# Kernel optimization log

Measured on AMD Instinct MI355X. Metric: run time of the kernel, lower is better.

Reference implementation:

```python
import jax, jax.numpy as jnp
import numpy as np

NEG_INF = -1e9
ALPHA = 0.2  # LeakyReLU slope


def gat_layer(x, adj, W, a_src, a_dst):
    # x: (N, F), adj: (N, N) bool, W: (F, H, D), a_src/a_dst: (H, D)
    h = jnp.einsum('nf,fhd->nhd', x, W)                 # (N, H, D)
    es = jnp.einsum('nhd,hd->nh', h, a_src)             # score from target node i
    ed = jnp.einsum('nhd,hd->nh', h, a_dst)             # score from neighbor j
    e = jax.nn.leaky_relu(es[:, None, :] + ed[None, :, :], ALPHA)  # (N, N, H)
    e = jnp.where(adj[:, :, None], e, NEG_INF)
    attn = jax.nn.softmax(e, axis=1)                    # softmax over neighbors j
    out = jnp.einsum('ijh,jhd->ihd', attn, h)           # (N, H, D)
    N, H, D = out.shape
    return out.reshape(N, H * D)                        # concat heads


def setup_inputs() -> dict:
    key = jax.random.key(0)
    ks = jax.random.split(key, 8)
    N, F, H1, D1, C = 4096, 512, 8, 8, 16
    node_matrix = jax.random.normal(ks[0], (N, F), dtype=jnp.float32)
    adj = jax.random.bernoulli(ks[1], 0.005, (N, N))
    adj = jnp.logical_or(adj, jnp.eye(N, dtype=bool))   # self-loops
    s1 = 1.0 / np.sqrt(F)
    s2 = 1.0 / np.sqrt(H1 * D1)
    return {
        'node_matrix': node_matrix,
        'adj_matrix': adj,
        'W1': jax.random.normal(ks[2], (F, H1, D1), dtype=jnp.float32) * s1,
        'a1_src': jax.random.normal(ks[3], (H1, D1), dtype=jnp.float32) * s1,
        'a1_dst': jax.random.normal(ks[4], (H1, D1), dtype=jnp.float32) * s1,
        'W2': jax.random.normal(ks[5], (H1 * D1, 1, C), dtype=jnp.float32) * s2,
        'a2_src': jax.random.normal(ks[6], (1, C), dtype=jnp.float32) * s2,
        'a2_dst': jax.random.normal(ks[7], (1, C), dtype=jnp.float32) * s2,
    }


def reference(node_matrix, adj_matrix, W1, a1_src, a1_dst, W2, a2_src, a2_dst):
    # dropout layers are identity in eval mode
    z1 = gat_layer(node_matrix, adj_matrix, W1, a1_src, a1_dst)  # (N, 64)
    a1 = jax.nn.elu(z1)
    z2 = gat_layer(a1, adj_matrix, W2, a2_src, a2_dst)           # (N, num_classes)
    return z2
```

## Files before the change

kernel.cpp:

```cpp
#include <hip/hip_runtime.h>

#define N_NODES 4096
#define F_IN    512
#define NH1     8
#define F1      64
#define C2      16
#define MAXDEG  128

#define GEMM_BLKS (N_NODES / 8)
#define SCAN_BLKS (N_NODES / 4)

__device__ __forceinline__ float wave_sum(float v) {
    for (int o = 32; o >= 1; o >>= 1) v += __shfl_xor(v, o, 64);
    return v;
}

__global__ void detect_width_kernel(const unsigned char* __restrict__ adj,
                                    int* __restrict__ flag) {
    __shared__ unsigned int cnts[4];
    __shared__ unsigned int mxv;
    int t = threadIdx.x;
    if (t < 4) cnts[t] = 0u;
    if (t == 0) mxv = 0u;
    __syncthreads();
    unsigned int c0 = 0, c1 = 0, c2 = 0, c3 = 0, m = 0;
    const uint4* p = (const uint4*)(adj) + t * 16;
    #pragma unroll
    for (int i = 0; i < 16; ++i) {
        uint4 q = p[i];
        unsigned int wd[4] = {q.x, q.y, q.z, q.w};
        #pragma unroll
        for (int k = 0; k < 4; ++k) {
            unsigned int v = wd[k];
            unsigned int b0 = v & 0xffu, b1 = (v >> 8) & 0xffu;
            unsigned int b2 = (v >> 16) & 0xffu, b3 = (v >> 24) & 0xffu;
            if (b0) { c0++; m = m > b0 ? m : b0; }
            if (b1) { c1++; m = m > b1 ? m : b1; }
            if (b2) { c2++; m = m > b2 ? m : b2; }
            if (b3) { c3++; m = m > b3 ? m : b3; }
        }
    }
    atomicAdd(&cnts[0], c0); atomicAdd(&cnts[1], c1);
    atomicAdd(&cnts[2], c2); atomicAdd(&cnts[3], c3);
    atomicMax(&mxv, m);
    __syncthreads();
    if (t == 0) {
        int w;
        if (cnts[1] + cnts[2] + cnts[3] == 0u)      w = 4;
        else if (cnts[0] == 0u && cnts[1] == 0u)    w = 4;
        else if (cnts[0] == 0u && cnts[2] == 0u)    w = 2;
        else if (mxv <= 1u)                          w = 1;
        else                                         w = 2;
        *flag = w;
    }
}

__global__ __launch_bounds__(256) void frontend_kernel(
        const unsigned char* __restrict__ adj, const int* __restrict__ flag,
        unsigned short* __restrict__ neigh, int* __restrict__ deg,
        const float* __restrict__ x, const float* __restrict__ W1,
        const float* __restrict__ asrc, const float* __restrict__ adst,
        float* __restrict__ h1, float* __restrict__ es, float* __restrict__ ed) {
    __shared__ __align__(16) float smem[4096 + 2 * 4096];
    __shared__ int scnt[4];
    const int t = threadIdx.x;
    const int wv = t >> 6;
    const int l = t & 63;

    if (blockIdx.x < GEMM_BLKS) {
        float* xs  = smem;
        float* wt0 = smem + 4096;
        float* wt1 = smem + 8192;
        const int row0 = blockIdx.x * 8;

        {
            const float4* src = (const float4*)(x + (size_t)row0 * F_IN);
            float4* dst = (float4*)xs;
            #pragma unroll
            for (int i = 0; i < 4; ++i) dst[t + i * 256] = src[t + i * 256];
        }
        const float4* w1v = (const float4*)W1;
        {
            float4* d = (float4*)wt0;
            #pragma unroll
            for (int i = 0; i < 4; ++i) d[t + i * 256] = w1v[t + i * 256];
        }

        const int c = t & 63;
        const int rq = t >> 6;
        float a0 = 0.f, a1 = 0.f;
        float* wcur = wt0;
        float* wnxt = wt1;
        for (int tile = 0; tile < 8; ++tile) {
            __syncthreads();
            float4 pf0, pf1, pf2, pf3;
            if (tile < 7) {
                const float4* s = w1v + (size_t)(tile + 1) * 1024;
                pf0 = s[t]; pf1 = s[t + 256]; pf2 = s[t + 512]; pf3 = s[t + 768];
            }
            const float4* xr0 = (const float4*)&xs[rq * F_IN + tile * 64];
            const float4* xr1 = (const float4*)&xs[(rq + 4) * F_IN + tile * 64];
            #pragma unroll
            for (int kk = 0; kk < 64; kk += 4) {
                float4 x0 = xr0[kk >> 2];
                float4 x1 = xr1[kk >> 2];
                float w0 = wcur[(kk + 0) * 64 + c];
                float w1 = wcur[(kk + 1) * 64 + c];
                float w2 = wcur[(kk + 2) * 64 + c];
                float w3 = wcur[(kk + 3) * 64 + c];
                a0 += x0.x * w0 + x0.y * w1 + x0.z * w2 + x0.w * w3;
                a1 += x1.x * w0 + x1.y * w1 + x1.z * w2 + x1.w * w3;
            }
            if (tile < 7) {
                float4* d = (float4*)wnxt;
                d[t] = pf0; d[t + 256] = pf1; d[t + 512] = pf2; d[t + 768] = pf3;
            }
            float* tmp = wcur; wcur = wnxt; wnxt = tmp;
        }

        const int n0 = row0 + rq;
        h1[(size_t)n0 * F1 + c] = a0;
        h1[(size_t)(n0 + 4) * F1 + c] = a1;
        float s0 = a0 * asrc[c], d0 = a0 * adst[c];
        float s1 = a1 * asrc[c], d1 = a1 * adst[c];
        s0 += __shfl_xor(s0, 1); s0 += __shfl_xor(s0, 2); s0 += __shfl_xor(s0, 4);
        d0 += __shfl_xor(d0, 1); d0 += __shfl_xor(d0, 2); d0 += __shfl_xor(d0, 4);
        s1 += __shfl_xor(s1, 1); s1 += __shfl_xor(s1, 2); s1 += __shfl_xor(s1, 4);
        d1 += __shfl_xor(d1, 1); d1 += __shfl_xor(d1, 2); d1 += __shfl_xor(d1, 4);
        if ((c & 7) == 0) {
            es[n0 * NH1 + (c >> 3)] = s0;
            ed[n0 * NH1 + (c >> 3)] = d0;
            es[(n0 + 4) * NH1 + (c >> 3)] = s1;
            ed[(n0 + 4) * NH1 + (c >> 3)] = d1;
        }
    } else {
        const int row = (blockIdx.x - GEMM_BLKS) * 4 + wv;
        int* cnt = scnt + wv;
        if (l == 0) *cnt = 0;
        const int w = *flag;
        unsigned short* outp = neigh + (size_t)row * MAXDEG;
        if (w == 1) {
            const uint4* p = (const uint4*)(adj + (size_t)row * N_NODES);
            uint4 v[4];
            #pragma unroll
            for (int i = 0; i < 4; ++i) v[i] = p[l + 64 * i];
            #pragma unroll
            for (int i = 0; i < 4; ++i) {
                if ((v[i].x | v[i].y | v[i].z | v[i].w) == 0u) continue;
                unsigned int wd[4] = {v[i].x, v[i].y, v[i].z, v[i].w};
                int base = (l + 64 * i) * 16;
                for (int q = 0; q < 4; ++q) {
                    unsigned int word = wd[q];
                    for (int bb = 0; bb < 4; ++bb) {
                        if ((word >> (8 * bb)) & 0xffu) {
                            int pos = atomicAdd(cnt, 1);
                            if (pos < MAXDEG) outp[pos] = (unsigned short)(base + q * 4 + bb);
                        }
                    }
                }
            }
        } else if (w == 2) {
            const uint4* p = (const uint4*)(adj + (size_t)row * N_NODES * 2);
            uint4 v[8];
            #pragma unroll
            for (int i = 0; i < 8; ++i) v[i] = p[l + 64 * i];
            #pragma unroll
            for (int i = 0; i < 8; ++i) {
                if ((v[i].x | v[i].y | v[i].z | v[i].w) == 0u) continue;
                unsigned int wd[4] = {v[i].x, v[i].y, v[i].z, v[i].w};
                int base = (l + 64 * i) * 8;
                for (int q = 0; q < 4; ++q) {
                    unsigned int word = wd[q];
                    if (word & 0xffffu) {
                        int pos = atomicAdd(cnt, 1);
                        if (pos < MAXDEG) outp[pos] = (unsigned short)(base + q * 2);
                    }
                    if (word >> 16) {
                        int pos = atomicAdd(cnt, 1);
                        if (pos < MAXDEG) outp[pos] = (unsigned short)(base + q * 2 + 1);
                    }
                }
            }
        } else {
            const uint4* p = (const uint4*)(adj + (size_t)row * N_NODES * 4);
            #pragma unroll
            for (int b = 0; b < 2; ++b) {
                uint4 v[8];
                #pragma unroll
                for (int i = 0; i < 8; ++i) v[i] = p[l + 64 * (b * 8 + i)];
                #pragma unroll
                for (int i = 0; i < 8; ++i) {
                    if ((v[i].x | v[i].y | v[i].z | v[i].w) == 0u) continue;
                    unsigned int wd[4] = {v[i].x, v[i].y, v[i].z, v[i].w};
                    int base = (l + 64 * (b * 8 + i)) * 4;
                    for (int q = 0; q < 4; ++q) {
                        if (wd[q]) {
                            int pos = atomicAdd(cnt, 1);
                            if (pos < MAXDEG) outp[pos] = (unsigned short)(base + q);
                        }
                    }
                }
            }
        }
        if (l == 0) deg[row] = min(*cnt, MAXDEG);
    }
}

__global__ __launch_bounds__(256) void attn1_kernel(
        const unsigned short* __restrict__ neigh, const int* __restrict__ deg,
        const float* __restrict__ h1, const float* __restrict__ es,
        const float* __restrict__ ed, const float* __restrict__ W2,
        const float* __restrict__ a2s, const float* __restrict__ a2d,
        float* __restrict__ h2, float* __restrict__ es2, float* __restrict__ ed2) {
    __shared__ unsigned short listA[4 * MAXDEG];
    __shared__ float arowA[4 * 64];
    __shared__ float pbufA[4 * 576];
    const int t = threadIdx.x;
    const int wv = t >> 6;
    const int l = t & 63;
    const int i = blockIdx.x * 4 + wv;
    unsigned short* list = listA + wv * MAXDEG;
    float* arow = arowA + wv * 64;
    float* pw   = pbufA + wv * 576;
    const int hq = l >> 3;

    const int K = deg[i];
    const unsigned short* lst = neigh + (size_t)i * MAXDEG;
    for (int j = l; j < MAXDEG; j += 64) list[j] = (j < K) ? lst[j] : (unsigned short)0;
    __builtin_amdgcn_wave_barrier();

    float plsum[NH1];
    #pragma unroll
    for (int h = 0; h < NH1; ++h) plsum[h] = 0.f;
    const float4 e0 = *(const float4*)(es + (size_t)i * NH1);
    const float4 e1 = *(const float4*)(es + (size_t)i * NH1 + 4);
    const float esi[NH1] = {e0.x, e0.y, e0.z, e0.w, e1.x, e1.y, e1.z, e1.w};
    float acc = 0.f;

    for (int t0 = 0; t0 < K; t0 += 64) {
        const int tc = min(64, K - t0);
        const bool valid = l < tc;
        const int j = valid ? (int)list[t0 + l] : 0;
        const float4 d0 = *(const float4*)(ed + (size_t)j * NH1);
        const float4 d1 = *(const float4*)(ed + (size_t)j * NH1 + 4);
        const float edv[NH1] = {d0.x, d0.y, d0.z, d0.w, d1.x, d1.y, d1.z, d1.w};
        #pragma unroll
        for (int h = 0; h < NH1; ++h) {
            float v = esi[h] + edv[h];
            v = (v >= 0.f) ? v : 0.2f * v;
            float p = valid ? __expf(v) : 0.f;
            plsum[h] += p;
            pw[l * 9 + h] = p;
        }
        __builtin_amdgcn_wave_barrier();
        const int tcPad = (tc + 7) & ~7;
        for (int u = 0; u < tcPad; u += 8) {
            #pragma unroll
            for (int vv = 0; vv < 8; ++vv) {
                int jn = (int)list[t0 + u + vv];
                acc += pw[(u + vv) * 9 + hq] * h1[(size_t)jn * F1 + l];
            }
        }
        __builtin_amdgcn_wave_barrier();
    }
    float lsum[NH1];
    #pragma unroll
    for (int h = 0; h < NH1; ++h) lsum[h] = wave_sum(plsum[h]);
    float o = acc / lsum[hq];
    float a1v = (o > 0.f) ? o : (__expf(o) - 1.f);

    arow[l] = a1v;
    __builtin_amdgcn_wave_barrier();
    const int cc = l & 15;
    const int kg = l >> 4;
    float hacc = 0.f;
    #pragma unroll
    for (int k = 0; k < 16; ++k)
        hacc += arow[kg * 16 + k] * W2[(kg * 16 + k) * C2 + cc];
    hacc += __shfl_xor(hacc, 16);
    hacc += __shfl_xor(hacc, 32);
    if (l < C2) h2[(size_t)i * C2 + l] = hacc;
    float s2 = hacc * a2s[cc];
    float d2 = hacc * a2d[cc];
    s2 += __shfl_xor(s2, 1); s2 += __shfl_xor(s2, 2);
    s2 += __shfl_xor(s2, 4); s2 += __shfl_xor(s2, 8);
    d2 += __shfl_xor(d2, 1); d2 += __shfl_xor(d2, 2);
    d2 += __shfl_xor(d2, 4); d2 += __shfl_xor(d2, 8);
    if (l == 0) { es2[i] = s2; ed2[i] = d2; }
}

__global__ __launch_bounds__(256) void attn2_kernel(
        const unsigned short* __restrict__ neigh, const int* __restrict__ deg,
        const float* __restrict__ h2, const float* __restrict__ es2,
        const float* __restrict__ ed2, float* __restrict__ out) {
    __shared__ unsigned short listA[4 * MAXDEG];
    __shared__ float pbufA[4 * 64];
    const int t = threadIdx.x;
    const int wv = t >> 6;
    const int l = t & 63;
    const int i = blockIdx.x * 4 + wv;
    unsigned short* list = listA + wv * MAXDEG;
    float* pb = pbufA + wv * 64;
    const int c = l & 15;
    const int g = l >> 4;

    const int K = deg[i];
    const unsigned short* lst = neigh + (size_t)i * MAXDEG;
    for (int j = l; j < MAXDEG; j += 64) list[j] = (j < K) ? lst[j] : (unsigned short)0;
    __builtin_amdgcn_wave_barrier();

    float plsum = 0.f, acc = 0.f;
    const float esi = es2[i];
    for (int t0 = 0; t0 < K; t0 += 64) {
        const int tc = min(64, K - t0);
        const bool valid = l < tc;
        const int j = valid ? (int)list[t0 + l] : 0;
        float v = esi + ed2[j];
        v = (v >= 0.f) ? v : 0.2f * v;
        float p = valid ? __expf(v) : 0.f;
        plsum += p;
        pb[l] = p;
        __builtin_amdgcn_wave_barrier();
        const int tcPad = (tc + 3) & ~3;
        for (int u = g; u < tcPad; u += 4) {
            int jn = (int)list[t0 + u];
            acc += pb[u] * h2[(size_t)jn * C2 + c];
        }
        __builtin_amdgcn_wave_barrier();
    }
    float lsum = wave_sum(plsum);
    acc += __shfl_xor(acc, 16);
    acc += __shfl_xor(acc, 32);
    if (l < C2) out[(size_t)i * C2 + l] = acc / lsum;
}

extern "C" void kernel_launch(void* const* d_in, const int* in_sizes, int n_in,
                              void* d_out, int out_size, void* d_ws, size_t ws_size,
                              hipStream_t stream) {
    const float* x           = (const float*)d_in[0];
    const unsigned char* adj = (const unsigned char*)d_in[1];
    const float* W1          = (const float*)d_in[2];
    const float* a1src       = (const float*)d_in[3];
    const float* a1dst       = (const float*)d_in[4];
    const float* W2          = (const float*)d_in[5];
    const float* a2src       = (const float*)d_in[6];
    const float* a2dst       = (const float*)d_in[7];
    float* out = (float*)d_out;

    char* ws = (char*)d_ws;
    size_t off = 0;
    int* flag = (int*)(ws + off);                 off += 256;
    unsigned short* neigh = (unsigned short*)(ws + off);
    off += (size_t)N_NODES * MAXDEG * 2;
    int* deg = (int*)(ws + off);                  off += (size_t)N_NODES * 4;
    float* h1 = (float*)(ws + off);               off += (size_t)N_NODES * F1 * 4;
    float* es1 = (float*)(ws + off);              off += (size_t)N_NODES * NH1 * 4;
    float* ed1 = (float*)(ws + off);              off += (size_t)N_NODES * NH1 * 4;
    float* h2 = (float*)(ws + off);               off += (size_t)N_NODES * C2 * 4;
    float* es2 = (float*)(ws + off);              off += (size_t)N_NODES * 4;
    float* ed2 = (float*)(ws + off);              off += (size_t)N_NODES * 4;

    hipLaunchKernelGGL(detect_width_kernel, dim3(1), dim3(256), 0, stream, adj, flag);
    hipLaunchKernelGGL(frontend_kernel, dim3(GEMM_BLKS + SCAN_BLKS), dim3(256), 0, stream,
                       adj, flag, neigh, deg, x, W1, a1src, a1dst, h1, es1, ed1);
    hipLaunchKernelGGL(attn1_kernel, dim3(N_NODES / 4), dim3(256), 0, stream,
                       neigh, deg, h1, es1, ed1, W2, a2src, a2dst, h2, es2, ed2);
    hipLaunchKernelGGL(attn2_kernel, dim3(N_NODES / 4), dim3(256), 0, stream,
                       neigh, deg, h2, es2, ed2, out);
}
```

Baseline: 145.9 us.

## Fold width detection into scan waves, widen GEMM tile, use shuffles for neighbor lists

Removes the separate single-block width-detection kernel. Each scan wave now redoes the detection itself by reading the first 4 KB of adj with wave votes, which saves one launch and its serialization at the cost of redundant reads. The GEMM blocks now handle 16 rows each, reusing each W tile across more rows, and use a single W buffer with an extra barrier instead of double buffering. The attention kernels drop their LDS copies of the neighbor list and broadcast indices and weights with __shfl, removing LDS traffic and wave barriers.

```diff
diff --git a/kernel.cpp b/kernel.cpp
--- a/kernel.cpp
+++ b/kernel.cpp
@@ -7,90 +7,72 @@
 #define C2      16
 #define MAXDEG  128
 
-#define GEMM_BLKS (N_NODES / 8)
-#define SCAN_BLKS (N_NODES / 4)
+#define GEMM_BLKS 256
+#define SCAN_BLKS 1024
 
 __device__ __forceinline__ float wave_sum(float v) {
     for (int o = 32; o >= 1; o >>= 1) v += __shfl_xor(v, o, 64);
     return v;
 }
 
-__global__ void detect_width_kernel(const unsigned char* __restrict__ adj,
-                                    int* __restrict__ flag) {
-    __shared__ unsigned int cnts[4];
-    __shared__ unsigned int mxv;
-    int t = threadIdx.x;
-    if (t < 4) cnts[t] = 0u;
-    if (t == 0) mxv = 0u;
-    __syncthreads();
-    unsigned int c0 = 0, c1 = 0, c2 = 0, c3 = 0, m = 0;
-    const uint4* p = (const uint4*)(adj) + t * 16;
+__device__ __forceinline__ int detect_width_wave(const unsigned char* __restrict__ adj,
+                                                 int l) {
+    bool nz0 = false, nz1 = false, nz2 = false, nz3 = false;
+    unsigned int mx = 0u;
+    const uint4* p = (const uint4*)adj;
     #pragma unroll
-    for (int i = 0; i < 16; ++i) {
-        uint4 q = p[i];
+    for (int i = 0; i < 4; ++i) {
+        uint4 q = p[l + 64 * i];
         unsigned int wd[4] = {q.x, q.y, q.z, q.w};
         #pragma unroll
         for (int k = 0; k < 4; ++k) {
             unsigned int v = wd[k];
             unsigned int b0 = v & 0xffu, b1 = (v >> 8) & 0xffu;
             unsigned int b2 = (v >> 16) & 0xffu, b3 = (v >> 24) & 0xffu;
-            if (b0) { c0++; m = m > b0 ? m : b0; }
-            if (b1) { c1++; m = m > b1 ? m : b1; }
-            if (b2) { c2++; m = m > b2 ? m : b2; }
-            if (b3) { c3++; m = m > b3 ? m : b3; }
+            if (b0) { nz0 = true; mx = mx > b0 ? mx : b0; }
+            if (b1) { nz1 = true; mx = mx > b1 ? mx : b1; }
+            if (b2) { nz2 = true; mx = mx > b2 ? mx : b2; }
+            if (b3) { nz3 = true; mx = mx > b3 ? mx : b3; }
         }
     }
-    atomicAdd(&cnts[0], c0); atomicAdd(&cnts[1], c1);
-    atomicAdd(&cnts[2], c2); atomicAdd(&cnts[3], c3);
-    atomicMax(&mxv, m);
-    __syncthreads();
-    if (t == 0) {
-        int w;
-        if (cnts[1] + cnts[2] + cnts[3] == 0u)      w = 4;
-        else if (cnts[0] == 0u && cnts[1] == 0u)    w = 4;
-        else if (cnts[0] == 0u && cnts[2] == 0u)    w = 2;
-        else if (mxv <= 1u)                          w = 1;
-        else                                         w = 2;
-        *flag = w;
-    }
+    const bool a0 = __any(nz0), a1 = __any(nz1), a2 = __any(nz2), a3 = __any(nz3);
+    const bool big = __any(mx > 1u);
+    if (!a1 && !a2 && !a3) return 4;
+    if (!a0 && !a1)        return 4;
+    if (!a0 && !a2)        return 2;
+    if (!big)              return 1;
+    return 2;
 }
 
 __global__ __launch_bounds__(256) void frontend_kernel(
-        const unsigned char* __restrict__ adj, const int* __restrict__ flag,
+        const unsigned char* __restrict__ adj,
         unsigned short* __restrict__ neigh, int* __restrict__ deg,
         const float* __restrict__ x, const float* __restrict__ W1,
         const float* __restrict__ asrc, const float* __restrict__ adst,
         float* __restrict__ h1, float* __restrict__ es, float* __restrict__ ed) {
-    __shared__ __align__(16) float smem[4096 + 2 * 4096];
+    __shared__ __align__(16) float smem[8192 + 4096];
     __shared__ int scnt[4];
     const int t = threadIdx.x;
     const int wv = t >> 6;
     const int l = t & 63;
 
     if (blockIdx.x < GEMM_BLKS) {
-        float* xs  = smem;
-        float* wt0 = smem + 4096;
-        float* wt1 = smem + 8192;
-        const int row0 = blockIdx.x * 8;
-
+        float* xs = smem;
+        float* wt = smem + 8192;
+        const int row0 = blockIdx.x * 16;
         {
             const float4* src = (const float4*)(x + (size_t)row0 * F_IN);
             float4* dst = (float4*)xs;
             #pragma unroll
-            for (int i = 0; i < 4; ++i) dst[t + i * 256] = src[t + i * 256];
+            for (int i = 0; i < 8; ++i) dst[t + i * 256] = src[t + i * 256];
         }
         const float4* w1v = (const float4*)W1;
-        {
-            float4* d = (float4*)wt0;
-            #pragma unroll
-            for (int i = 0; i < 4; ++i) d[t + i * 256] = w1v[t + i * 256];
-        }
-
-        const int c = t & 63;
-        const int rq = t >> 6;
-        float a0 = 0.f, a1 = 0.f;
-        float* wcur = wt0;
-        float* wnxt = wt1;
+        float4* wtv = (float4*)wt;
+        #pragma unroll
+        for (int i = 0; i < 4; ++i) wtv[t + i * 256] = w1v[t + i * 256];
+
+        const int c = l;
+        float a0 = 0.f, a1 = 0.f, a2 = 0.f, a3 = 0.f;
         for (int tile = 0; tile < 8; ++tile) {
             __syncthreads();
             float4 pf0, pf1, pf2, pf3;
@@ -98,46 +80,50 @@
                 const float4* s = w1v + (size_t)(tile + 1) * 1024;
                 pf0 = s[t]; pf1 = s[t + 256]; pf2 = s[t + 512]; pf3 = s[t + 768];
             }
-            const float4* xr0 = (const float4*)&xs[rq * F_IN + tile * 64];
-            const float4* xr1 = (const float4*)&xs[(rq + 4) * F_IN + tile * 64];
+            const float4* xr0 = (const float4*)&xs[(wv     ) * F_IN + tile * 64];
+            const float4* xr1 = (const float4*)&xs[(wv +  4) * F_IN + tile * 64];
+            const float4* xr2 = (const float4*)&xs[(wv +  8) * F_IN + tile * 64];
+            const float4* xr3 = (const float4*)&xs[(wv + 12) * F_IN + tile * 64];
             #pragma unroll
             for (int kk = 0; kk < 64; kk += 4) {
                 float4 x0 = xr0[kk >> 2];
                 float4 x1 = xr1[kk >> 2];
-                float w0 = wcur[(kk + 0) * 64 + c];
-                float w1 = wcur[(kk + 1) * 64 + c];
-                float w2 = wcur[(kk + 2) * 64 + c];
-                float w3 = wcur[(kk + 3) * 64 + c];
+                float4 x2 = xr2[kk >> 2];
+                float4 x3 = xr3[kk >> 2];
+                float w0 = wt[(kk + 0) * 64 + c];
+                float w1 = wt[(kk + 1) * 64 + c];
+                float w2 = wt[(kk + 2) * 64 + c];
+                float w3 = wt[(kk + 3) * 64 + c];
                 a0 += x0.x * w0 + x0.y * w1 + x0.z * w2 + x0.w * w3;
                 a1 += x1.x * w0 + x1.y * w1 + x1.z * w2 + x1.w * w3;
-            }
+                a2 += x2.x * w0 + x2.y * w1 + x2.z * w2 + x2.w * w3;
+                a3 += x3.x * w0 + x3.y * w1 + x3.z * w2 + x3.w * w3;
+            }
+            __syncthreads();
             if (tile < 7) {
-                float4* d = (float4*)wnxt;
-                d[t] = pf0; d[t + 256] = pf1; d[t + 512] = pf2; d[t + 768] = pf3;
-            }
-            float* tmp = wcur; wcur = wnxt; wnxt = tmp;
-        }
-
-        const int n0 = row0 + rq;
-        h1[(size_t)n0 * F1 + c] = a0;
-        h1[(size_t)(n0 + 4) * F1 + c] = a1;
-        float s0 = a0 * asrc[c], d0 = a0 * adst[c];
-        float s1 = a1 * asrc[c], d1 = a1 * adst[c];
-        s0 += __shfl_xor(s0, 1); s0 += __shfl_xor(s0, 2); s0 += __shfl_xor(s0, 4);
-        d0 += __shfl_xor(d0, 1); d0 += __shfl_xor(d0, 2); d0 += __shfl_xor(d0, 4);
-        s1 += __shfl_xor(s1, 1); s1 += __shfl_xor(s1, 2); s1 += __shfl_xor(s1, 4);
-        d1 += __shfl_xor(d1, 1); d1 += __shfl_xor(d1, 2); d1 += __shfl_xor(d1, 4);
-        if ((c & 7) == 0) {
-            es[n0 * NH1 + (c >> 3)] = s0;
-            ed[n0 * NH1 + (c >> 3)] = d0;
-            es[(n0 + 4) * NH1 + (c >> 3)] = s1;
-            ed[(n0 + 4) * NH1 + (c >> 3)] = d1;
+                wtv[t] = pf0; wtv[t + 256] = pf1;
+                wtv[t + 512] = pf2; wtv[t + 768] = pf3;
+            }
+        }
+        float acc[4] = {a0, a1, a2, a3};
+        #pragma unroll
+        for (int r = 0; r < 4; ++r) {
+            const int n = row0 + wv + 4 * r;
+            h1[(size_t)n * F1 + c] = acc[r];
+            float s = acc[r] * asrc[c];
+            float d = acc[r] * adst[c];
+            s += __shfl_xor(s, 1); s += __shfl_xor(s, 2); s += __shfl_xor(s, 4);
+            d += __shfl_xor(d, 1); d += __shfl_xor(d, 2); d += __shfl_xor(d, 4);
+            if ((c & 7) == 0) {
+                es[n * NH1 + (c >> 3)] = s;
+                ed[n * NH1 + (c >> 3)] = d;
+            }
         }
     } else {
+        const int w = detect_width_wave(adj, l);
         const int row = (blockIdx.x - GEMM_BLKS) * 4 + wv;
         int* cnt = scnt + wv;
         if (l == 0) *cnt = 0;
-        const int w = *flag;
         unsigned short* outp = neigh + (size_t)row * MAXDEG;
         if (w == 1) {
             const uint4* p = (const uint4*)(adj + (size_t)row * N_NODES);
@@ -212,22 +198,18 @@
         const float* __restrict__ ed, const float* __restrict__ W2,
         const float* __restrict__ a2s, const float* __restrict__ a2d,
         float* __restrict__ h2, float* __restrict__ es2, float* __restrict__ ed2) {
-    __shared__ unsigned short listA[4 * MAXDEG];
+    __shared__ float pbufA[4 * 576];
     __shared__ float arowA[4 * 64];
-    __shared__ float pbufA[4 * 576];
     const int t = threadIdx.x;
     const int wv = t >> 6;
     const int l = t & 63;
     const int i = blockIdx.x * 4 + wv;
-    unsigned short* list = listA + wv * MAXDEG;
+    float* pw   = pbufA + wv * 576;
     float* arow = arowA + wv * 64;
-    float* pw   = pbufA + wv * 576;
     const int hq = l >> 3;
 
     const int K = deg[i];
     const unsigned short* lst = neigh + (size_t)i * MAXDEG;
-    for (int j = l; j < MAXDEG; j += 64) list[j] = (j < K) ? lst[j] : (unsigned short)0;
-    __builtin_amdgcn_wave_barrier();
 
     float plsum[NH1];
     #pragma unroll
@@ -240,10 +222,11 @@
     for (int t0 = 0; t0 < K; t0 += 64) {
         const int tc = min(64, K - t0);
         const bool valid = l < tc;
-        const int j = valid ? (int)list[t0 + l] : 0;
-        const float4 d0 = *(const float4*)(ed + (size_t)j * NH1);
-        const float4 d1 = *(const float4*)(ed + (size_t)j * NH1 + 4);
-        const float edv[NH1] = {d0.x, d0.y, d0.z, d0.w, d1.x, d1.y, d1.z, d1.w};
+        const int j = valid ? (int)lst[t0 + l] : 0;
+        const float4 d0v = *(const float4*)(ed + (size_t)j * NH1);
+        const float4 d1v = *(const float4*)(ed + (size_t)j * NH1 + 4);
+        const float edv[NH1] = {d0v.x, d0v.y, d0v.z, d0v.w,
+                                d1v.x, d1v.y, d1v.z, d1v.w};
         #pragma unroll
         for (int h = 0; h < NH1; ++h) {
             float v = esi[h] + edv[h];
@@ -257,8 +240,9 @@
         for (int u = 0; u < tcPad; u += 8) {
             #pragma unroll
             for (int vv = 0; vv < 8; ++vv) {
-                int jn = (int)list[t0 + u + vv];
-                acc += pw[(u + vv) * 9 + hq] * h1[(size_t)jn * F1 + l];
+                const int slot = u + vv;
+                const int jn = __shfl(j, slot);
+                acc += pw[slot * 9 + hq] * h1[(size_t)jn * F1 + l];
             }
         }
         __builtin_amdgcn_wave_barrier();
@@ -293,40 +277,32 @@
         const unsigned short* __restrict__ neigh, const int* __restrict__ deg,
         const float* __restrict__ h2, const float* __restrict__ es2,
         const float* __restrict__ ed2, float* __restrict__ out) {
-    __shared__ unsigned short listA[4 * MAXDEG];
-    __shared__ float pbufA[4 * 64];
     const int t = threadIdx.x;
     const int wv = t >> 6;
     const int l = t & 63;
     const int i = blockIdx.x * 4 + wv;
-    unsigned short* list = listA + wv * MAXDEG;
-    float* pb = pbufA + wv * 64;
     const int c = l & 15;
     const int g = l >> 4;
 
     const int K = deg[i];
     const unsigned short* lst = neigh + (size_t)i * MAXDEG;
-    for (int j = l; j < MAXDEG; j += 64) list[j] = (j < K) ? lst[j] : (unsigned short)0;
-    __builtin_amdgcn_wave_barrier();
 
     float plsum = 0.f, acc = 0.f;
     const float esi = es2[i];
     for (int t0 = 0; t0 < K; t0 += 64) {
         const int tc = min(64, K - t0);
         const bool valid = l < tc;
-        const int j = valid ? (int)list[t0 + l] : 0;
+        const int j = valid ? (int)lst[t0 + l] : 0;
         float v = esi + ed2[j];
         v = (v >= 0.f) ? v : 0.2f * v;
         float p = valid ? __expf(v) : 0.f;
         plsum += p;
-        pb[l] = p;
-        __builtin_amdgcn_wave_barrier();
         const int tcPad = (tc + 3) & ~3;
         for (int u = g; u < tcPad; u += 4) {
-            int jn = (int)list[t0 + u];
-            acc += pb[u] * h2[(size_t)jn * C2 + c];
-        }
-        __builtin_amdgcn_wave_barrier();
+            const int jn = __shfl(j, u);
+            const float pv = __shfl(p, u);
+            acc += pv * h2[(size_t)jn * C2 + c];
+        }
     }
     float lsum = wave_sum(plsum);
     acc += __shfl_xor(acc, 16);
@@ -349,20 +325,19 @@
 
     char* ws = (char*)d_ws;
     size_t off = 0;
-    int* flag = (int*)(ws + off);                 off += 256;
+    off += 256;
     unsigned short* neigh = (unsigned short*)(ws + off);
     off += (size_t)N_NODES * MAXDEG * 2;
-    int* deg = (int*)(ws + off);                  off += (size_t)N_NODES * 4;
-    float* h1 = (float*)(ws + off);               off += (size_t)N_NODES * F1 * 4;
-    float* es1 = (float*)(ws + off);              off += (size_t)N_NODES * NH1 * 4;
-    float* ed1 = (float*)(ws + off);              off += (size_t)N_NODES * NH1 * 4;
-    float* h2 = (float*)(ws + off);               off += (size_t)N_NODES * C2 * 4;
-    float* es2 = (float*)(ws + off);              off += (size_t)N_NODES * 4;
-    float* ed2 = (float*)(ws + off);              off += (size_t)N_NODES * 4;
-
-    hipLaunchKernelGGL(detect_width_kernel, dim3(1), dim3(256), 0, stream, adj, flag);
+    int* deg = (int*)(ws + off);                      off += (size_t)N_NODES * 4;
+    float* h1 = (float*)(ws + off);                   off += (size_t)N_NODES * F1 * 4;
+    float* es1 = (float*)(ws + off);                  off += (size_t)N_NODES * NH1 * 4;
+    float* ed1 = (float*)(ws + off);                  off += (size_t)N_NODES * NH1 * 4;
+    float* h2 = (float*)(ws + off);                   off += (size_t)N_NODES * C2 * 4;
+    float* es2 = (float*)(ws + off);                  off += (size_t)N_NODES * 4;
+    float* ed2 = (float*)(ws + off);                  off += (size_t)N_NODES * 4;
+
     hipLaunchKernelGGL(frontend_kernel, dim3(GEMM_BLKS + SCAN_BLKS), dim3(256), 0, stream,
-                       adj, flag, neigh, deg, x, W1, a1src, a1dst, h1, es1, ed1);
+                       adj, neigh, deg, x, W1, a1src, a1dst, h1, es1, ed1);
     hipLaunchKernelGGL(attn1_kernel, dim3(N_NODES / 4), dim3(256), 0, stream,
                        neigh, deg, h1, es1, ed1, W2, a2src, a2dst, h2, es2, ed2);
     hipLaunchKernelGGL(attn2_kernel, dim3(N_NODES / 4), dim3(256), 0, stream,
```

Result: faster. 142.2 us (-2.6%).
